# Kernel tuning notes

Measured on AMD Instinct MI355X. Metric: run time of the kernel, lower is better.

Reference implementation:

```python
import jax, jax.numpy as jnp
import numpy as np

P = 3  # cubic B-spline degree
N_KNOTS = 8
LATENT = 32


def _de_boor(x, t, c):
    # Vectorized de Boor: digitize -> gather control points -> 3-level blend.
    k = jnp.digitize(x, t) - 1
    d = [c[j + k - P] for j in range(P + 1)]
    for r in range(1, P + 1):
        for j in range(P, r - 1, -1):
            alpha = (x - t[j + k - P]) / (t[j + 1 + k - r] - t[j + k - P])
            d[j] = (1.0 - alpha) * d[j - 1] + alpha * d[j]
    return d[P]


def setup_inputs() -> dict:
    key = jax.random.key(0)
    ks = jax.random.split(key, 10)
    f32 = jnp.float32
    x = jax.random.uniform(ks[0], (256, 256, 256), dtype=f32)
    a = jax.random.uniform(ks[1], (1,), dtype=f32)
    # Dense params (lecun-normal-ish init, zero bias like flax defaults)
    W1 = jax.random.normal(ks[2], (1, LATENT), f32)
    b1 = jnp.zeros((LATENT,), f32)
    W2 = jax.random.normal(ks[3], (LATENT, LATENT), f32) / np.sqrt(LATENT)
    b2 = jnp.zeros((LATENT,), f32)
    Ww = jax.random.normal(ks[4], (LATENT, N_KNOTS + 1), f32) / np.sqrt(LATENT)
    bw = jnp.zeros((N_KNOTS + 1,), f32)
    Wk = jax.random.normal(ks[5], (LATENT, N_KNOTS - 1), f32) / np.sqrt(LATENT)
    bk = jnp.zeros((N_KNOTS - 1,), f32)
    return {"x": x, "a": a, "W1": W1, "b1": b1, "W2": W2, "b2": b2,
            "Ww": Ww, "bw": bw, "Wk": Wk, "bk": bk}


def reference(x, a, W1, b1, W2, b2, Ww, bw, Wk, bk):
    a_vec = jnp.atleast_1d(a)
    net = jnp.sin(a_vec @ W1 + b1)
    net = jnp.sin(net @ W2 + b2)
    w = net @ Ww + bw                      # (n_knots+1,)
    kraw = net @ Wk + bk                   # (n_knots-1,)
    kpos = jnp.concatenate([jnp.zeros((1,), x.dtype),
                            jnp.cumsum(jax.nn.softmax(kraw))])
    w = jnp.concatenate([jnp.zeros((1,), x.dtype), w])
    ak = jnp.concatenate([jnp.zeros((3,), x.dtype), kpos, jnp.ones((3,), x.dtype)])
    xp = jnp.clip(x / jnp.sqrt(jnp.asarray(3.0, x.dtype)), 0.0, 1.0 - 0.0001)
    return _de_boor(xp, ak, w)
```

## Files before the change

### kernel.cpp

```cpp
#include <hip/hip_runtime.h>

__global__ void build_params_kernel(const float* __restrict__ a,
                                    const float* __restrict__ W1, const float* __restrict__ b1,
                                    const float* __restrict__ W2, const float* __restrict__ b2,
                                    const float* __restrict__ Ww, const float* __restrict__ bw,
                                    const float* __restrict__ Wk, const float* __restrict__ bk,
                                    float* __restrict__ ws) {
    __shared__ float net1[32];
    __shared__ float net2[32];
    __shared__ float w9[9];
    __shared__ float kraw[7];
    const int tid = threadIdx.x;
    const float av = a[0];
    if (tid < 32) net1[tid] = sinf(av * W1[tid] + b1[tid]);
    __syncthreads();
    if (tid < 32) {
        float s = b2[tid];
        for (int j = 0; j < 32; ++j) s += net1[j] * W2[j * 32 + tid];
        net2[tid] = sinf(s);
    }
    __syncthreads();
    if (tid < 9) {
        float s = bw[tid];
        for (int j = 0; j < 32; ++j) s += net2[j] * Ww[j * 9 + tid];
        w9[tid] = s;
    } else if (tid >= 16 && tid < 23) {
        const int i = tid - 16;
        float s = bk[i];
        for (int j = 0; j < 32; ++j) s += net2[j] * Wk[j * 7 + i];
        kraw[i] = s;
    }
    __syncthreads();
    if (tid == 0) {
        float mx = kraw[0];
        for (int i = 1; i < 7; ++i) mx = fmaxf(mx, kraw[i]);
        float e[7];
        float sum = 0.f;
        for (int i = 0; i < 7; ++i) { e[i] = expf(kraw[i] - mx); sum += e[i]; }
        const float invsum = 1.f / sum;
        float t[14];
        t[0] = t[1] = t[2] = t[3] = 0.f;
        float cs = 0.f;
        for (int i = 0; i < 7; ++i) { cs += e[i] * invsum; t[4 + i] = cs; }
        t[11] = t[12] = t[13] = 1.f;
        float w10[10];
        w10[0] = 0.f;
        for (int i = 0; i < 9; ++i) w10[1 + i] = w9[i];
        for (int i = 0; i < 6; ++i) ws[i] = t[4 + i];
        ws[6] = 0.f; ws[7] = 0.f;
        for (int kk = 0; kk < 7; ++kk) {
            const int k = kk + 3;
            float d[4][4];
            for (int j = 0; j < 4; ++j) {
                d[j][0] = w10[k - 3 + j];
                d[j][1] = 0.f; d[j][2] = 0.f; d[j][3] = 0.f;
            }
            for (int r = 1; r <= 3; ++r) {
                for (int j = 3; j >= r; --j) {
                    const float t0 = t[j + k - 3];
                    const float t1 = t[j + 1 + k - r];
                    const float den = t1 - t0;
                    const float invd = (den != 0.f) ? (1.f / den) : 0.f;
                    const float a1 = invd;
                    const float a0 = (t[k] - t0) * invd;
                    float nd[4];
                    for (int i = 0; i < 4; ++i) {
                        const float diff = d[j][i] - d[j - 1][i];
                        nd[i] = d[j - 1][i] + a0 * diff;
                    }
                    for (int i = 0; i < 3; ++i) {
                        const float diff = d[j][i] - d[j - 1][i];
                        nd[i + 1] += a1 * diff;
                    }
                    for (int i = 0; i < 4; ++i) d[j][i] = nd[i];
                }
            }
            ws[8 + 4 * kk + 0] = d[3][0];
            ws[8 + 4 * kk + 1] = d[3][1];
            ws[8 + 4 * kk + 2] = d[3][2];
            ws[8 + 4 * kk + 3] = d[3][3];
        }
    }
}

__device__ __forceinline__ float eval_one(float xi, const float cs[6], const float4* tbl) {
    float xp = fminf(fmaxf(xi * 0.57735026918962576f, 0.0f), 0.9999f);
    int kk = 0;
    float tk = 0.f;
#pragma unroll
    for (int i = 0; i < 6; ++i) {
        if (xp >= cs[i]) { kk = i + 1; tk = cs[i]; }
    }
    const float s = xp - tk;
    const float4 cf = tbl[kk];
    return fmaf(fmaf(fmaf(cf.w, s, cf.z), s, cf.y), s, cf.x);
}

__global__ __launch_bounds__(256) void spline_eval_kernel(const float4* __restrict__ x,
                                                          const float* __restrict__ ws,
                                                          float4* __restrict__ out,
                                                          int n4) {
    __shared__ float4 tbl[7];
    if (threadIdx.x < 7) {
        const float4* src = (const float4*)(ws + 8);
        tbl[threadIdx.x] = src[threadIdx.x];
    }
    float cs[6];
#pragma unroll
    for (int i = 0; i < 6; ++i) cs[i] = ws[i];
    __syncthreads();
    const int idx = blockIdx.x * 256 + threadIdx.x;
    if (idx >= n4) return;
    const float4 xv = x[idx];
    float4 r;
    r.x = eval_one(xv.x, cs, tbl);
    r.y = eval_one(xv.y, cs, tbl);
    r.z = eval_one(xv.z, cs, tbl);
    r.w = eval_one(xv.w, cs, tbl);
    out[idx] = r;
}

extern "C" void kernel_launch(void* const* d_in, const int* in_sizes, int n_in,
                              void* d_out, int out_size, void* d_ws, size_t ws_size,
                              hipStream_t stream) {
    const float* x  = (const float*)d_in[0];
    const float* a  = (const float*)d_in[1];
    const float* W1 = (const float*)d_in[2];
    const float* b1 = (const float*)d_in[3];
    const float* W2 = (const float*)d_in[4];
    const float* b2 = (const float*)d_in[5];
    const float* Ww = (const float*)d_in[6];
    const float* bw = (const float*)d_in[7];
    const float* Wk = (const float*)d_in[8];
    const float* bk = (const float*)d_in[9];
    float* ws  = (float*)d_ws;
    float* out = (float*)d_out;

    build_params_kernel<<<1, 64, 0, stream>>>(a, W1, b1, W2, b2, Ww, bw, Wk, bk, ws);

    const int n4 = out_size / 4;
    const int blocks = (n4 + 255) / 256;
    spline_eval_kernel<<<blocks, 256, 0, stream>>>((const float4*)x, ws, (float4*)out, n4);
}
```

Before: 135.4 us.

## Fuse parameter MLP into spline eval kernel with grid-stride loop

Merges the single-block parameter-building kernel into the evaluation kernel: each of 2048 blocks recomputes the tiny MLP, softmax knots and per-interval cubic coefficients (now spread across 7 threads) in shared memory, then runs a grid-stride loop over the input. This removes a kernel launch and the dependency on a workspace round trip. The cost is redundant prologue work in every block and a fixed grid size that may change occupancy and memory-level parallelism for the 16M-element streaming pass.

```diff
diff --git a/kernel.cpp b/kernel.cpp
--- a/kernel.cpp
+++ b/kernel.cpp
@@ -1,123 +1,109 @@
 #include <hip/hip_runtime.h>
 
-__global__ void build_params_kernel(const float* __restrict__ a,
-                                    const float* __restrict__ W1, const float* __restrict__ b1,
-                                    const float* __restrict__ W2, const float* __restrict__ b2,
-                                    const float* __restrict__ Ww, const float* __restrict__ bw,
-                                    const float* __restrict__ Wk, const float* __restrict__ bk,
-                                    float* __restrict__ ws) {
+__global__ __launch_bounds__(256) void nsff_fused_kernel(
+    const float4* __restrict__ x, float4* __restrict__ out, int n4,
+    const float* __restrict__ a,
+    const float* __restrict__ W1, const float* __restrict__ b1,
+    const float* __restrict__ W2, const float* __restrict__ b2,
+    const float* __restrict__ Ww, const float* __restrict__ bw,
+    const float* __restrict__ Wk, const float* __restrict__ bk) {
     __shared__ float net1[32];
     __shared__ float net2[32];
-    __shared__ float w9[9];
-    __shared__ float kraw[7];
+    __shared__ float w9s[9];
+    __shared__ float kraws[7];
+    __shared__ float tsh[14];
+    __shared__ float w10s[10];
+    __shared__ float4 tbl[7];
+    __shared__ float csh[6];
+
     const int tid = threadIdx.x;
-    const float av = a[0];
-    if (tid < 32) net1[tid] = sinf(av * W1[tid] + b1[tid]);
+
+    if (tid < 32) net1[tid] = sinf(a[0] * W1[tid] + b1[tid]);
     __syncthreads();
     if (tid < 32) {
         float s = b2[tid];
+#pragma unroll
         for (int j = 0; j < 32; ++j) s += net1[j] * W2[j * 32 + tid];
         net2[tid] = sinf(s);
     }
     __syncthreads();
     if (tid < 9) {
         float s = bw[tid];
+#pragma unroll
         for (int j = 0; j < 32; ++j) s += net2[j] * Ww[j * 9 + tid];
-        w9[tid] = s;
+        w9s[tid] = s;
     } else if (tid >= 16 && tid < 23) {
         const int i = tid - 16;
         float s = bk[i];
+#pragma unroll
         for (int j = 0; j < 32; ++j) s += net2[j] * Wk[j * 7 + i];
-        kraw[i] = s;
+        kraws[i] = s;
     }
     __syncthreads();
     if (tid == 0) {
-        float mx = kraw[0];
-        for (int i = 1; i < 7; ++i) mx = fmaxf(mx, kraw[i]);
-        float e[7];
-        float sum = 0.f;
-        for (int i = 0; i < 7; ++i) { e[i] = expf(kraw[i] - mx); sum += e[i]; }
+        float mx = kraws[0];
+        for (int i = 1; i < 7; ++i) mx = fmaxf(mx, kraws[i]);
+        float e[7], sum = 0.f;
+        for (int i = 0; i < 7; ++i) { e[i] = expf(kraws[i] - mx); sum += e[i]; }
         const float invsum = 1.f / sum;
-        float t[14];
-        t[0] = t[1] = t[2] = t[3] = 0.f;
+        tsh[0] = tsh[1] = tsh[2] = tsh[3] = 0.f;
         float cs = 0.f;
-        for (int i = 0; i < 7; ++i) { cs += e[i] * invsum; t[4 + i] = cs; }
-        t[11] = t[12] = t[13] = 1.f;
-        float w10[10];
-        w10[0] = 0.f;
-        for (int i = 0; i < 9; ++i) w10[1 + i] = w9[i];
-        for (int i = 0; i < 6; ++i) ws[i] = t[4 + i];
-        ws[6] = 0.f; ws[7] = 0.f;
-        for (int kk = 0; kk < 7; ++kk) {
-            const int k = kk + 3;
-            float d[4][4];
-            for (int j = 0; j < 4; ++j) {
-                d[j][0] = w10[k - 3 + j];
-                d[j][1] = 0.f; d[j][2] = 0.f; d[j][3] = 0.f;
+        for (int i = 0; i < 7; ++i) { cs += e[i] * invsum; tsh[4 + i] = cs; }
+        tsh[11] = tsh[12] = tsh[13] = 1.f;
+        w10s[0] = 0.f;
+        for (int i = 0; i < 9; ++i) w10s[1 + i] = w9s[i];
+        for (int i = 0; i < 6; ++i) csh[i] = tsh[4 + i];
+    }
+    __syncthreads();
+    if (tid < 7) {
+        const int k = tid + 3;
+        float d[4][4];
+        for (int j = 0; j < 4; ++j) {
+            d[j][0] = w10s[k - 3 + j];
+            d[j][1] = 0.f; d[j][2] = 0.f; d[j][3] = 0.f;
+        }
+        for (int r = 1; r <= 3; ++r) {
+            for (int j = 3; j >= r; --j) {
+                const float t0 = tsh[j + k - 3];
+                const float t1 = tsh[j + 1 + k - r];
+                const float den = t1 - t0;
+                const float invd = (den != 0.f) ? (1.f / den) : 0.f;
+                const float a0 = (tsh[k] - t0) * invd;
+                float nd[4];
+                for (int i = 0; i < 4; ++i) nd[i] = d[j - 1][i] + a0 * (d[j][i] - d[j - 1][i]);
+                for (int i = 0; i < 3; ++i) nd[i + 1] += invd * (d[j][i] - d[j - 1][i]);
+                for (int i = 0; i < 4; ++i) d[j][i] = nd[i];
             }
-            for (int r = 1; r <= 3; ++r) {
-                for (int j = 3; j >= r; --j) {
-                    const float t0 = t[j + k - 3];
-                    const float t1 = t[j + 1 + k - r];
-                    const float den = t1 - t0;
-                    const float invd = (den != 0.f) ? (1.f / den) : 0.f;
-                    const float a1 = invd;
-                    const float a0 = (t[k] - t0) * invd;
-                    float nd[4];
-                    for (int i = 0; i < 4; ++i) {
-                        const float diff = d[j][i] - d[j - 1][i];
-                        nd[i] = d[j - 1][i] + a0 * diff;
-                    }
-                    for (int i = 0; i < 3; ++i) {
-                        const float diff = d[j][i] - d[j - 1][i];
-                        nd[i + 1] += a1 * diff;
-                    }
-                    for (int i = 0; i < 4; ++i) d[j][i] = nd[i];
-                }
-            }
-            ws[8 + 4 * kk + 0] = d[3][0];
-            ws[8 + 4 * kk + 1] = d[3][1];
-            ws[8 + 4 * kk + 2] = d[3][2];
-            ws[8 + 4 * kk + 3] = d[3][3];
         }
+        tbl[tid] = make_float4(d[3][0], d[3][1], d[3][2], d[3][3]);
     }
-}
+    __syncthreads();
 
-__device__ __forceinline__ float eval_one(float xi, const float cs[6], const float4* tbl) {
-    float xp = fminf(fmaxf(xi * 0.57735026918962576f, 0.0f), 0.9999f);
-    int kk = 0;
-    float tk = 0.f;
-#pragma unroll
-    for (int i = 0; i < 6; ++i) {
-        if (xp >= cs[i]) { kk = i + 1; tk = cs[i]; }
-    }
-    const float s = xp - tk;
-    const float4 cf = tbl[kk];
-    return fmaf(fmaf(fmaf(cf.w, s, cf.z), s, cf.y), s, cf.x);
-}
-
-__global__ __launch_bounds__(256) void spline_eval_kernel(const float4* __restrict__ x,
-                                                          const float* __restrict__ ws,
-                                                          float4* __restrict__ out,
-                                                          int n4) {
-    __shared__ float4 tbl[7];
-    if (threadIdx.x < 7) {
-        const float4* src = (const float4*)(ws + 8);
-        tbl[threadIdx.x] = src[threadIdx.x];
-    }
     float cs[6];
 #pragma unroll
-    for (int i = 0; i < 6; ++i) cs[i] = ws[i];
-    __syncthreads();
-    const int idx = blockIdx.x * 256 + threadIdx.x;
-    if (idx >= n4) return;
-    const float4 xv = x[idx];
-    float4 r;
-    r.x = eval_one(xv.x, cs, tbl);
-    r.y = eval_one(xv.y, cs, tbl);
-    r.z = eval_one(xv.z, cs, tbl);
-    r.w = eval_one(xv.w, cs, tbl);
-    out[idx] = r;
+    for (int i = 0; i < 6; ++i) cs[i] = csh[i];
+
+    const int stride = gridDim.x * 256;
+#pragma unroll 2
+    for (int idx = blockIdx.x * 256 + tid; idx < n4; idx += stride) {
+        const float4 xv = x[idx];
+        float4 r;
+#pragma unroll
+        for (int c = 0; c < 4; ++c) {
+            const float xi = (&xv.x)[c];
+            float xp = fminf(fmaxf(xi * 0.57735026918962576f, 0.0f), 0.9999f);
+            int kk = 0;
+            float tk = 0.f;
+#pragma unroll
+            for (int i = 0; i < 6; ++i) {
+                if (xp >= cs[i]) { kk = i + 1; tk = cs[i]; }
+            }
+            const float s = xp - tk;
+            const float4 cf = tbl[kk];
+            (&r.x)[c] = fmaf(fmaf(fmaf(cf.w, s, cf.z), s, cf.y), s, cf.x);
+        }
+        out[idx] = r;
+    }
 }
 
 extern "C" void kernel_launch(void* const* d_in, const int* in_sizes, int n_in,
@@ -133,12 +119,10 @@
     const float* bw = (const float*)d_in[7];
     const float* Wk = (const float*)d_in[8];
     const float* bk = (const float*)d_in[9];
-    float* ws  = (float*)d_ws;
     float* out = (float*)d_out;
 
-    build_params_kernel<<<1, 64, 0, stream>>>(a, W1, b1, W2, b2, Ww, bw, Wk, bk, ws);
-
     const int n4 = out_size / 4;
-    const int blocks = (n4 + 255) / 256;
-    spline_eval_kernel<<<blocks, 256, 0, stream>>>((const float4*)x, ws, (float4*)out, n4);
+    const int blocks = 2048;
+    nsff_fused_kernel<<<blocks, 256, 0, stream>>>((const float4*)x, (float4*)out, n4,
+                                                  a, W1, b1, W2, b2, Ww, bw, Wk, bk);
 }
```

New measurement: 131.1 us. 3.2% less time.
